# Optimization experiments

Measured on AMD Instinct MI355X. Metric: run time of the kernel, lower is better.

Reference implementation:

```python
import jax, jax.numpy as jnp
import numpy as np
from jax import lax

B, T, I, H, L = 256, 4096, 6, 64, 4


def setup_inputs() -> dict:
    key = jax.random.key(0)
    ks = jax.random.split(key, 8)
    s = 1.0 / np.sqrt(H)  # PyTorch LSTM init scale
    return {
        "x": jax.random.normal(ks[0], (B, T, I), jnp.float32),
        "Wih0": jax.random.uniform(ks[1], (4 * H, I), jnp.float32, -s, s),
        "Wih_rest": jax.random.uniform(ks[2], (L - 1, 4 * H, H), jnp.float32, -s, s),
        "Whh": jax.random.uniform(ks[3], (L, 4 * H, H), jnp.float32, -s, s),
        "bih": jax.random.uniform(ks[4], (L, 4 * H), jnp.float32, -s, s),
        "bhh": jax.random.uniform(ks[5], (L, 4 * H), jnp.float32, -s, s),
        "fc_w": jax.random.uniform(ks[6], (1, H), jnp.float32, -s, s),
        "fc_b": jax.random.uniform(ks[7], (1,), jnp.float32, -s, s),
    }


def _lstm_layer(seq_tbi, Wih_l, Whh_l, b_l):
    # seq_tbi: [T, B, in], time-major. Precompute input projections for all t.
    gx = jnp.einsum('tbi,gi->tbg', seq_tbi, Wih_l) + b_l  # [T, B, 4H]
    batch = seq_tbi.shape[1]
    h0 = jnp.zeros((batch, H), seq_tbi.dtype)
    c0 = jnp.zeros((batch, H), seq_tbi.dtype)

    def step(carry, gxt):
        h, c = carry
        g = gxt + h @ Whh_l.T  # [B, 4H]
        i, f, gg, o = jnp.split(g, 4, axis=-1)  # PyTorch gate order: i,f,g,o
        c = jax.nn.sigmoid(f) * c + jax.nn.sigmoid(i) * jnp.tanh(gg)
        h = jax.nn.sigmoid(o) * jnp.tanh(c)
        return (h, c), h

    _, ys = lax.scan(step, (h0, c0), gx)
    return ys  # [T, B, H]


def reference(x, Wih0, Wih_rest, Whh, bih, bhh, fc_w, fc_b):
    # x: [B, T, I] (batch_first). Dropout(0.2) between layers is inactive (eval).
    seq = jnp.transpose(x, (1, 0, 2))  # time-major [T, B, I]
    for l in range(L):
        Wih_l = Wih0 if l == 0 else Wih_rest[l - 1]
        seq = _lstm_layer(seq, Wih_l, Whh[l], bih[l] + bhh[l])
    last = seq[-1]                      # out[:, -1, :] -> [B, H]
    out = jax.nn.relu(last) @ fc_w.T + fc_b  # [B, 1]
    return out
```

## Files before the change

### kernel.cpp

```cpp
#include <hip/hip_runtime.h>
#include <cstddef>

#define BB 256
#define TT 4096
#define HH 64
#define NT 256
#define CH 8
#define NCH (TT / CH)
#define NGB 16
#define LOG2E 1.442695041f

typedef __attribute__((ext_vector_type(8))) short short8;
typedef __attribute__((ext_vector_type(4))) short short4v;
typedef __attribute__((ext_vector_type(4))) float floatx4;

__device__ int g_flags[3 * NGB];
__global__ void zero_flags_kernel() { g_flags[threadIdx.x] = 0; }

__device__ __forceinline__ floatx4 mfma16(short8 a, short8 b, floatx4 c) {
    return __builtin_amdgcn_mfma_f32_16x16x32_bf16(a, b, c, 0, 0, 0);
}
__device__ __forceinline__ float frcp(float x) { return __builtin_amdgcn_rcpf(x); }
__device__ __forceinline__ void lds_barrier() {
    asm volatile("s_waitcnt lgkmcnt(0)\n\ts_barrier" ::: "memory");
}
__device__ __forceinline__ void bf16split(float v, short& hi, short& lo) {
    unsigned u  = __float_as_uint(v);
    unsigned hu = u & 0xffff0000u;
    hi = (short)(hu >> 16);
    float r = v - __uint_as_float(hu);
    lo = (short)(__float_as_uint(r) >> 16);
}

__global__ __attribute__((amdgpu_flat_work_group_size(NT, NT), amdgpu_waves_per_eu(1)))
void lstm_mfma(const float* __restrict__ xg,
               const float* __restrict__ Wih0,
               const float* __restrict__ WihR,
               const float* __restrict__ Whh4,
               const float* __restrict__ bih4,
               const float* __restrict__ bhh4,
               float* __restrict__ seq)
{
    const int bid = blockIdx.x;
    const int l   = bid >> 4;
    const int gb  = bid & 15;
    const int b0  = gb << 4;
    const bool FIRST = (l == 0);
    const bool LAST  = (l == 3);
    const float* Wih = FIRST ? Wih0 : (WihR + (size_t)(l - 1) * 256 * HH);
    const float* Whh = Whh4 + (size_t)l * 256 * HH;
    int* const fin  = &g_flags[(l - 1) * NGB + gb];
    int* const fout = &g_flags[l * NGB + gb];

    const int tid = threadIdx.x;
    const int w   = tid >> 6;
    const int ln  = tid & 63;
    const int n   = ln & 15;
    const int g4  = ln >> 4;
    const int k0  = (w << 4) + (g4 << 2);

    __shared__ __align__(16) unsigned short xhi[2][CH][16][72];
    __shared__ __align__(16) unsigned short xlo[2][CH][16][72];
    __shared__ __align__(16) unsigned short hhi[2][16][72];
    __shared__ __align__(16) unsigned short hlo[2][16][72];

    short8 whi[4][4], wlo[4][4];
#pragma unroll
    for (int q = 0; q < 4; ++q) {
        const float sc = (q == 2) ? (-2.f * LOG2E) : (-LOG2E);
        const int gr = (q << 6) + (w << 4) + n;
#pragma unroll
        for (int s = 0; s < 4; ++s) {
            const int kb = s * 32 + g4 * 8;
            float wv[8];
#pragma unroll
            for (int i = 0; i < 8; ++i) {
                const int k = kb + i;
                float v;
                if (k < 64)      v = Whh[gr * 64 + k];
                else if (!FIRST) v = Wih[gr * 64 + (k - 64)];
                else             v = (k - 64 < 6) ? Wih[gr * 6 + (k - 64)] : 0.f;
                wv[i] = v * sc;
            }
            short8 hi, lo;
#pragma unroll
            for (int i = 0; i < 8; ++i) { short a, b2; bf16split(wv[i], a, b2); hi[i] = a; lo[i] = b2; }
            whi[q][s] = hi; wlo[q][s] = lo;
        }
    }
    floatx4 bias[4];
#pragma unroll
    for (int q = 0; q < 4; ++q) {
        const float sc = (q == 2) ? (-2.f * LOG2E) : (-LOG2E);
#pragma unroll
        for (int r = 0; r < 4; ++r) {
            const int gr = (q << 6) + k0 + r;
            bias[q][r] = (bih4[l * 256 + gr] + bhh4[l * 256 + gr]) * sc;
        }
    }

    {
        unsigned short* p0 = &xhi[0][0][0][0];
        for (int i = tid; i < 2 * CH * 16 * 72; i += NT) { p0[i] = 0; (&xlo[0][0][0][0])[i] = 0; }
        unsigned short* p1 = &hhi[0][0][0];
        for (int i = tid; i < 2 * 16 * 72; i += NT) { p1[i] = 0; (&hlo[0][0][0])[i] = 0; }
    }
    __syncthreads();

    const int tt = tid >> 5;
    const int sn = (tid >> 1) & 15;
    const int kh = (tid & 1) * 32;
    const int ttf = tid >> 4;
    const int nf  = tid & 15;

    if (!FIRST) {
        if (tid == 0)
            while (__hip_atomic_load(fin, __ATOMIC_ACQUIRE, __HIP_MEMORY_SCOPE_AGENT) < 1)
                __builtin_amdgcn_s_sleep(8);
        __syncthreads();
        const float* src = seq + ((size_t)(0 * CH + tt) * BB + b0 + sn) * HH + kh;
        floatx4 pv[8];
#pragma unroll
        for (int m = 0; m < 8; ++m) pv[m] = ((const floatx4*)src)[m];
#pragma unroll
        for (int m = 0; m < 4; ++m) {
            short8 hi8, lo8;
#pragma unroll
            for (int i = 0; i < 8; ++i) {
                const float v = (i < 4) ? pv[2 * m][i] : pv[2 * m + 1][i - 4];
                short a, b2; bf16split(v, a, b2); hi8[i] = a; lo8[i] = b2;
            }
            *(short8*)&xhi[0][tt][sn][kh + 8 * m] = hi8;
            *(short8*)&xlo[0][tt][sn][kh + 8 * m] = lo8;
        }
    } else if (tid < 128) {
        const float* sx = xg + ((size_t)(b0 + nf) * TT + ttf) * 6;
#pragma unroll
        for (int i = 0; i < 6; ++i) {
            short a, b2; bf16split(sx[i], a, b2);
            xhi[0][ttf][nf][i] = (unsigned short)a;
            xlo[0][ttf][nf][i] = (unsigned short)b2;
        }
    }
    float c0 = 0.f, c1 = 0.f, c2 = 0.f, c3 = 0.f;
    __syncthreads();

    for (int ck = 0; ck < NCH; ++ck) {
        const int buf = ck & 1;
        const bool pfv = (ck + 1 < NCH);
        if (!FIRST && pfv) {
            if (tid == 0)
                while (__hip_atomic_load(fin, __ATOMIC_ACQUIRE, __HIP_MEMORY_SCOPE_AGENT) < ck + 2)
                    __builtin_amdgcn_s_sleep(8);
            __syncthreads();
        }
        floatx4 pv[8];
        float xv[6];

#pragma unroll
        for (int ph = 0; ph < CH; ++ph) {
            const int t = ck * CH + ph;
            if (ph == 0 && pfv) {
                if (!FIRST) {
                    const float* src = seq + ((size_t)((ck + 1) * CH + tt) * BB + b0 + sn) * HH + kh;
#pragma unroll
                    for (int m = 0; m < 8; ++m) pv[m] = ((const floatx4*)src)[m];
                } else if (tid < 128) {
                    const float* sx = xg + ((size_t)(b0 + nf) * TT + (ck + 1) * CH + ttf) * 6;
#pragma unroll
                    for (int i = 0; i < 6; ++i) xv[i] = sx[i];
                }
            }

            const int hb = (t + 1) & 1;
            const short8 bh0 = *(const short8*)&hhi[hb][n][g4 * 8];
            const short8 bh1 = *(const short8*)&hhi[hb][n][32 + g4 * 8];
            const short8 bl0 = *(const short8*)&hlo[hb][n][g4 * 8];
            const short8 bl1 = *(const short8*)&hlo[hb][n][32 + g4 * 8];
            const short8 bx0 = *(const short8*)&xhi[buf][ph][n][g4 * 8];
            const short8 bx1 = *(const short8*)&xhi[buf][ph][n][32 + g4 * 8];
            const short8 by0 = *(const short8*)&xlo[buf][ph][n][g4 * 8];
            const short8 by1 = *(const short8*)&xlo[buf][ph][n][32 + g4 * 8];

            floatx4 a0 = bias[0], a1 = bias[1], a2 = bias[2], a3 = bias[3];
#define TERM(bq0, bq1, bq2, bq3, W) \
            a0 = mfma16(W[0][0], bq0, a0); a1 = mfma16(W[1][0], bq0, a1); \
            a2 = mfma16(W[2][0], bq0, a2); a3 = mfma16(W[3][0], bq0, a3); \
            a0 = mfma16(W[0][1], bq1, a0); a1 = mfma16(W[1][1], bq1, a1); \
            a2 = mfma16(W[2][1], bq1, a2); a3 = mfma16(W[3][1], bq1, a3); \
            a0 = mfma16(W[0][2], bq2, a0); a1 = mfma16(W[1][2], bq2, a1); \
            a2 = mfma16(W[2][2], bq2, a2); a3 = mfma16(W[3][2], bq2, a3); \
            a0 = mfma16(W[0][3], bq3, a0); a1 = mfma16(W[1][3], bq3, a1); \
            a2 = mfma16(W[2][3], bq3, a2); a3 = mfma16(W[3][3], bq3, a3);
            TERM(bh0, bh1, bx0, bx1, whi)
            TERM(bl0, bl1, by0, by1, whi)
            TERM(bh0, bh1, bx0, bx1, wlo)
#undef TERM

            floatx4 hv4;
            short4v h4hi, h4lo;
#define UNIT(r, cr) { \
            const float si = frcp(1.f + exp2f(a0[r])); \
            const float sf = frcp(1.f + exp2f(a1[r])); \
            const float tg = fmaf(2.f, frcp(1.f + exp2f(a2[r])), -1.f); \
            const float so = frcp(1.f + exp2f(a3[r])); \
            cr = fmaf(sf, cr, si * tg); \
            const float tc = fmaf(2.f, frcp(1.f + exp2f(cr * (-2.f * LOG2E))), -1.f); \
            const float hv = so * tc; \
            hv4[r] = hv; \
            short ha, hbs; bf16split(hv, ha, hbs); h4hi[r] = ha; h4lo[r] = hbs; }
            UNIT(0, c0) UNIT(1, c1) UNIT(2, c2) UNIT(3, c3)
#undef UNIT

            *(short4v*)&hhi[t & 1][n][k0] = h4hi;
            *(short4v*)&hlo[t & 1][n][k0] = h4lo;
            if (!LAST || t == TT - 1)
                *(floatx4*)(seq + ((size_t)t * BB + b0 + n) * HH + k0) = hv4;

            if (pfv) {
                if (!FIRST) {
                    if (ph >= 4) {
                        const int m = ph - 4;
                        short8 hi8, lo8;
#pragma unroll
                        for (int i = 0; i < 8; ++i) {
                            const float v = (i < 4) ? pv[2 * m][i] : pv[2 * m + 1][i - 4];
                            short a, b2; bf16split(v, a, b2); hi8[i] = a; lo8[i] = b2;
                        }
                        *(short8*)&xhi[1 - buf][tt][sn][kh + 8 * m] = hi8;
                        *(short8*)&xlo[1 - buf][tt][sn][kh + 8 * m] = lo8;
                    }
                } else if (ph == 2 && tid < 128) {
#pragma unroll
                    for (int i = 0; i < 6; ++i) {
                        short a, b2; bf16split(xv[i], a, b2);
                        xhi[1 - buf][ttf][nf][i] = (unsigned short)a;
                        xlo[1 - buf][ttf][nf][i] = (unsigned short)b2;
                    }
                }
            }

            if (ph < CH - 1) lds_barrier();
            else             __syncthreads();
        }
        if (!LAST && tid == 0)
            __hip_atomic_store(fout, ck + 1, __ATOMIC_RELEASE, __HIP_MEMORY_SCOPE_AGENT);
    }
}

__global__ __launch_bounds__(256)
void fc_kernel(const float* __restrict__ seq, const float* __restrict__ fcw,
               const float* __restrict__ fcb, float* __restrict__ out)
{
    __shared__ float w[HH];
    const int tid = threadIdx.x;
    if (tid < HH) w[tid] = fcw[tid];
    __syncthreads();
    const float* h = &seq[((size_t)(TT - 1) * BB + tid) * HH];
    float s = fcb[0];
#pragma unroll
    for (int jj = 0; jj < HH; ++jj)
        s = fmaf(fmaxf(h[jj], 0.f), w[jj], s);
    out[tid] = s;
}

extern "C" void kernel_launch(void* const* d_in, const int* in_sizes, int n_in,
                              void* d_out, int out_size, void* d_ws, size_t ws_size,
                              hipStream_t stream) {
    const float* x    = (const float*)d_in[0];
    const float* Wih0 = (const float*)d_in[1];
    const float* WihR = (const float*)d_in[2];
    const float* Whh  = (const float*)d_in[3];
    const float* bih  = (const float*)d_in[4];
    const float* bhh  = (const float*)d_in[5];
    const float* fcw  = (const float*)d_in[6];
    const float* fcb  = (const float*)d_in[7];
    float* out = (float*)d_out;
    float* seq = (float*)d_ws;

    zero_flags_kernel<<<dim3(1), dim3(3 * NGB), 0, stream>>>();
    lstm_mfma<<<dim3(4 * NGB), dim3(NT), 0, stream>>>(x, Wih0, WihR, Whh, bih, bhh, seq);
    fc_kernel<<<dim3(1), dim3(256), 0, stream>>>(seq, fcw, fcb, out);
}
```

Baseline: 4.470 ms.

## Batch input-projection MFMAs for four timesteps ahead of the recurrent chain

Each 8-step chunk is split into two groups of four. For each group the input-projection MFMAs (the x-term products) for all four timesteps are computed up front into accumulators. Only the 24 recurrent h-term MFMAs per step then stay on the serial critical path, which is meant to shorten per-step latency in the recurrence. In exchange, 16 extra floatx4 accumulators (64 VGPRs) stay live across steps, which raises register pressure and may cause spills or lower occupancy.

```diff
diff --git a/kernel.cpp b/kernel.cpp
--- a/kernel.cpp
+++ b/kernel.cpp
@@ -158,90 +158,113 @@
         float xv[6];
 
 #pragma unroll
-        for (int ph = 0; ph < CH; ++ph) {
-            const int t = ck * CH + ph;
-            if (ph == 0 && pfv) {
-                if (!FIRST) {
-                    const float* src = seq + ((size_t)((ck + 1) * CH + tt) * BB + b0 + sn) * HH + kh;
-#pragma unroll
-                    for (int m = 0; m < 8; ++m) pv[m] = ((const floatx4*)src)[m];
-                } else if (tid < 128) {
-                    const float* sx = xg + ((size_t)(b0 + nf) * TT + (ck + 1) * CH + ttf) * 6;
-#pragma unroll
-                    for (int i = 0; i < 6; ++i) xv[i] = sx[i];
-                }
+        for (int scn = 0; scn < 2; ++scn) {
+            floatx4 xacc[4][4];
+#pragma unroll
+            for (int s = 0; s < 4; ++s) {
+                const int ph = scn * 4 + s;
+                const short8 bx0 = *(const short8*)&xhi[buf][ph][n][g4 * 8];
+                const short8 bx1 = *(const short8*)&xhi[buf][ph][n][32 + g4 * 8];
+                const short8 by0 = *(const short8*)&xlo[buf][ph][n][g4 * 8];
+                const short8 by1 = *(const short8*)&xlo[buf][ph][n][32 + g4 * 8];
+                floatx4 q0 = bias[0], q1 = bias[1], q2 = bias[2], q3 = bias[3];
+                q0 = mfma16(whi[0][2], bx0, q0); q1 = mfma16(whi[1][2], bx0, q1);
+                q2 = mfma16(whi[2][2], bx0, q2); q3 = mfma16(whi[3][2], bx0, q3);
+                q0 = mfma16(whi[0][3], bx1, q0); q1 = mfma16(whi[1][3], bx1, q1);
+                q2 = mfma16(whi[2][3], bx1, q2); q3 = mfma16(whi[3][3], bx1, q3);
+                q0 = mfma16(wlo[0][2], bx0, q0); q1 = mfma16(wlo[1][2], bx0, q1);
+                q2 = mfma16(wlo[2][2], bx0, q2); q3 = mfma16(wlo[3][2], bx0, q3);
+                q0 = mfma16(wlo[0][3], bx1, q0); q1 = mfma16(wlo[1][3], bx1, q1);
+                q2 = mfma16(wlo[2][3], bx1, q2); q3 = mfma16(wlo[3][3], bx1, q3);
+                q0 = mfma16(whi[0][2], by0, q0); q1 = mfma16(whi[1][2], by0, q1);
+                q2 = mfma16(whi[2][2], by0, q2); q3 = mfma16(whi[3][2], by0, q3);
+                q0 = mfma16(whi[0][3], by1, q0); q1 = mfma16(whi[1][3], by1, q1);
+                q2 = mfma16(whi[2][3], by1, q2); q3 = mfma16(whi[3][3], by1, q3);
+                xacc[s][0] = q0; xacc[s][1] = q1; xacc[s][2] = q2; xacc[s][3] = q3;
             }
 
-            const int hb = (t + 1) & 1;
-            const short8 bh0 = *(const short8*)&hhi[hb][n][g4 * 8];
-            const short8 bh1 = *(const short8*)&hhi[hb][n][32 + g4 * 8];
-            const short8 bl0 = *(const short8*)&hlo[hb][n][g4 * 8];
-            const short8 bl1 = *(const short8*)&hlo[hb][n][32 + g4 * 8];
-            const short8 bx0 = *(const short8*)&xhi[buf][ph][n][g4 * 8];
-            const short8 bx1 = *(const short8*)&xhi[buf][ph][n][32 + g4 * 8];
-            const short8 by0 = *(const short8*)&xlo[buf][ph][n][g4 * 8];
-            const short8 by1 = *(const short8*)&xlo[buf][ph][n][32 + g4 * 8];
-
-            floatx4 a0 = bias[0], a1 = bias[1], a2 = bias[2], a3 = bias[3];
-#define TERM(bq0, bq1, bq2, bq3, W) \
-            a0 = mfma16(W[0][0], bq0, a0); a1 = mfma16(W[1][0], bq0, a1); \
-            a2 = mfma16(W[2][0], bq0, a2); a3 = mfma16(W[3][0], bq0, a3); \
-            a0 = mfma16(W[0][1], bq1, a0); a1 = mfma16(W[1][1], bq1, a1); \
-            a2 = mfma16(W[2][1], bq1, a2); a3 = mfma16(W[3][1], bq1, a3); \
-            a0 = mfma16(W[0][2], bq2, a0); a1 = mfma16(W[1][2], bq2, a1); \
-            a2 = mfma16(W[2][2], bq2, a2); a3 = mfma16(W[3][2], bq2, a3); \
-            a0 = mfma16(W[0][3], bq3, a0); a1 = mfma16(W[1][3], bq3, a1); \
-            a2 = mfma16(W[2][3], bq3, a2); a3 = mfma16(W[3][3], bq3, a3);
-            TERM(bh0, bh1, bx0, bx1, whi)
-            TERM(bl0, bl1, by0, by1, whi)
-            TERM(bh0, bh1, bx0, bx1, wlo)
-#undef TERM
-
-            floatx4 hv4;
-            short4v h4hi, h4lo;
-#define UNIT(r, cr) { \
-            const float si = frcp(1.f + exp2f(a0[r])); \
-            const float sf = frcp(1.f + exp2f(a1[r])); \
-            const float tg = fmaf(2.f, frcp(1.f + exp2f(a2[r])), -1.f); \
-            const float so = frcp(1.f + exp2f(a3[r])); \
-            cr = fmaf(sf, cr, si * tg); \
-            const float tc = fmaf(2.f, frcp(1.f + exp2f(cr * (-2.f * LOG2E))), -1.f); \
-            const float hv = so * tc; \
-            hv4[r] = hv; \
-            short ha, hbs; bf16split(hv, ha, hbs); h4hi[r] = ha; h4lo[r] = hbs; }
-            UNIT(0, c0) UNIT(1, c1) UNIT(2, c2) UNIT(3, c3)
-#undef UNIT
-
-            *(short4v*)&hhi[t & 1][n][k0] = h4hi;
-            *(short4v*)&hlo[t & 1][n][k0] = h4lo;
-            if (!LAST || t == TT - 1)
-                *(floatx4*)(seq + ((size_t)t * BB + b0 + n) * HH + k0) = hv4;
-
-            if (pfv) {
-                if (!FIRST) {
-                    if (ph >= 4) {
-                        const int m = ph - 4;
-                        short8 hi8, lo8;
-#pragma unroll
-                        for (int i = 0; i < 8; ++i) {
-                            const float v = (i < 4) ? pv[2 * m][i] : pv[2 * m + 1][i - 4];
-                            short a, b2; bf16split(v, a, b2); hi8[i] = a; lo8[i] = b2;
-                        }
-                        *(short8*)&xhi[1 - buf][tt][sn][kh + 8 * m] = hi8;
-                        *(short8*)&xlo[1 - buf][tt][sn][kh + 8 * m] = lo8;
-                    }
-                } else if (ph == 2 && tid < 128) {
-#pragma unroll
-                    for (int i = 0; i < 6; ++i) {
-                        short a, b2; bf16split(xv[i], a, b2);
-                        xhi[1 - buf][ttf][nf][i] = (unsigned short)a;
-                        xlo[1 - buf][ttf][nf][i] = (unsigned short)b2;
+#pragma unroll
+            for (int s = 0; s < 4; ++s) {
+                const int ph = scn * 4 + s;
+                const int t = ck * CH + ph;
+                if (ph == 0 && pfv) {
+                    if (!FIRST) {
+                        const float* src = seq + ((size_t)((ck + 1) * CH + tt) * BB + b0 + sn) * HH + kh;
+#pragma unroll
+                        for (int m = 0; m < 8; ++m) pv[m] = ((const floatx4*)src)[m];
+                    } else if (tid < 128) {
+                        const float* sx = xg + ((size_t)(b0 + nf) * TT + (ck + 1) * CH + ttf) * 6;
+#pragma unroll
+                        for (int i = 0; i < 6; ++i) xv[i] = sx[i];
                     }
                 }
+
+                const int hb = (t + 1) & 1;
+                const short8 bh0 = *(const short8*)&hhi[hb][n][g4 * 8];
+                const short8 bh1 = *(const short8*)&hhi[hb][n][32 + g4 * 8];
+                const short8 bl0 = *(const short8*)&hlo[hb][n][g4 * 8];
+                const short8 bl1 = *(const short8*)&hlo[hb][n][32 + g4 * 8];
+
+                floatx4 a0 = xacc[s][0], a1 = xacc[s][1], a2 = xacc[s][2], a3 = xacc[s][3];
+                a0 = mfma16(whi[0][0], bh0, a0); a1 = mfma16(whi[1][0], bh0, a1);
+                a2 = mfma16(whi[2][0], bh0, a2); a3 = mfma16(whi[3][0], bh0, a3);
+                a0 = mfma16(whi[0][1], bh1, a0); a1 = mfma16(whi[1][1], bh1, a1);
+                a2 = mfma16(whi[2][1], bh1, a2); a3 = mfma16(whi[3][1], bh1, a3);
+                a0 = mfma16(wlo[0][0], bh0, a0); a1 = mfma16(wlo[1][0], bh0, a1);
+                a2 = mfma16(wlo[2][0], bh0, a2); a3 = mfma16(wlo[3][0], bh0, a3);
+                a0 = mfma16(wlo[0][1], bh1, a0); a1 = mfma16(wlo[1][1], bh1, a1);
+                a2 = mfma16(wlo[2][1], bh1, a2); a3 = mfma16(wlo[3][1], bh1, a3);
+                a0 = mfma16(whi[0][0], bl0, a0); a1 = mfma16(whi[1][0], bl0, a1);
+                a2 = mfma16(whi[2][0], bl0, a2); a3 = mfma16(whi[3][0], bl0, a3);
+                a0 = mfma16(whi[0][1], bl1, a0); a1 = mfma16(whi[1][1], bl1, a1);
+                a2 = mfma16(whi[2][1], bl1, a2); a3 = mfma16(whi[3][1], bl1, a3);
+
+                floatx4 hv4;
+                short4v h4hi, h4lo;
+#define UNIT(r, cr) { \
+                const float si = frcp(1.f + exp2f(a0[r])); \
+                const float sf = frcp(1.f + exp2f(a1[r])); \
+                const float tg = fmaf(2.f, frcp(1.f + exp2f(a2[r])), -1.f); \
+                const float so = frcp(1.f + exp2f(a3[r])); \
+                cr = fmaf(sf, cr, si * tg); \
+                const float tc = fmaf(2.f, frcp(1.f + exp2f(cr * (-2.f * LOG2E))), -1.f); \
+                const float hv = so * tc; \
+                hv4[r] = hv; \
+                short ha, hbs; bf16split(hv, ha, hbs); h4hi[r] = ha; h4lo[r] = hbs; }
+                UNIT(0, c0) UNIT(1, c1) UNIT(2, c2) UNIT(3, c3)
+#undef UNIT
+
+                *(short4v*)&hhi[t & 1][n][k0] = h4hi;
+                *(short4v*)&hlo[t & 1][n][k0] = h4lo;
+                if (!LAST || t == TT - 1)
+                    *(floatx4*)(seq + ((size_t)t * BB + b0 + n) * HH + k0) = hv4;
+
+                if (pfv) {
+                    if (!FIRST) {
+                        if (ph >= 4) {
+                            const int m = ph - 4;
+                            short8 hi8, lo8;
+#pragma unroll
+                            for (int i = 0; i < 8; ++i) {
+                                const float v = (i < 4) ? pv[2 * m][i] : pv[2 * m + 1][i - 4];
+                                short a, b2; bf16split(v, a, b2); hi8[i] = a; lo8[i] = b2;
+                            }
+                            *(short8*)&xhi[1 - buf][tt][sn][kh + 8 * m] = hi8;
+                            *(short8*)&xlo[1 - buf][tt][sn][kh + 8 * m] = lo8;
+                        }
+                    } else if (ph == 2 && tid < 128) {
+#pragma unroll
+                        for (int i = 0; i < 6; ++i) {
+                            short a, b2; bf16split(xv[i], a, b2);
+                            xhi[1 - buf][ttf][nf][i] = (unsigned short)a;
+                            xlo[1 - buf][ttf][nf][i] = (unsigned short)b2;
+                        }
+                    }
+                }
+
+                if (ph < CH - 1) lds_barrier();
+                else             __syncthreads();
             }
-
-            if (ph < CH - 1) lds_barrier();
-            else             __syncthreads();
         }
         if (!LAST && tid == 0)
             __hip_atomic_store(fout, ck + 1, __ATOMIC_RELEASE, __HIP_MEMORY_SCOPE_AGENT);
```

New measurement: 4.658 ms. 1.04x slower.

## Pack two 16-sample batch groups per workgroup with 512 threads and halve chunk size

Applied to the files above, without the earlier changes.

Each workgroup now runs two independent 16-batch recurrences (two groups of four waves), cutting the grid from 64 to 32 blocks with two waves per SIMD. The idea is to let one group's MFMA and transcendental latency hide behind the other's on the same CU, since the serial recurrence leaves each SIMD mostly idle. Chunk size drops from 8 to 4 timesteps, and the next-chunk conversion is split into a hi pass and a lo pass on separate phases. The risk is that barriers now synchronize both groups together, and register pressure rises with two waves per EU, which could slow each step.

```diff
diff --git a/kernel.cpp b/kernel.cpp
--- a/kernel.cpp
+++ b/kernel.cpp
@@ -4,17 +4,17 @@
 #define BB 256
 #define TT 4096
 #define HH 64
-#define NT 256
-#define CH 8
+#define NT 512
+#define CH 4
 #define NCH (TT / CH)
-#define NGB 16
+#define NPAIR 8
 #define LOG2E 1.442695041f
 
 typedef __attribute__((ext_vector_type(8))) short short8;
 typedef __attribute__((ext_vector_type(4))) short short4v;
 typedef __attribute__((ext_vector_type(4))) float floatx4;
 
-__device__ int g_flags[3 * NGB];
+__device__ int g_flags[3 * NPAIR];
 __global__ void zero_flags_kernel() { g_flags[threadIdx.x] = 0; }
 
 __device__ __forceinline__ floatx4 mfma16(short8 a, short8 b, floatx4 c) {
@@ -32,7 +32,7 @@
     lo = (short)(__float_as_uint(r) >> 16);
 }
 
-__global__ __attribute__((amdgpu_flat_work_group_size(NT, NT), amdgpu_waves_per_eu(1)))
+__global__ __attribute__((amdgpu_flat_work_group_size(NT, NT), amdgpu_waves_per_eu(2)))
 void lstm_mfma(const float* __restrict__ xg,
                const float* __restrict__ Wih0,
                const float* __restrict__ WihR,
@@ -42,27 +42,29 @@
                float* __restrict__ seq)
 {
     const int bid = blockIdx.x;
-    const int l   = bid >> 4;
-    const int gb  = bid & 15;
-    const int b0  = gb << 4;
+    const int l   = bid >> 3;
+    const int gb  = bid & 7;
     const bool FIRST = (l == 0);
     const bool LAST  = (l == 3);
     const float* Wih = FIRST ? Wih0 : (WihR + (size_t)(l - 1) * 256 * HH);
     const float* Whh = Whh4 + (size_t)l * 256 * HH;
-    int* const fin  = &g_flags[(l - 1) * NGB + gb];
-    int* const fout = &g_flags[l * NGB + gb];
-
-    const int tid = threadIdx.x;
-    const int w   = tid >> 6;
-    const int ln  = tid & 63;
-    const int n   = ln & 15;
-    const int g4  = ln >> 4;
-    const int k0  = (w << 4) + (g4 << 2);
-
-    __shared__ __align__(16) unsigned short xhi[2][CH][16][72];
-    __shared__ __align__(16) unsigned short xlo[2][CH][16][72];
-    __shared__ __align__(16) unsigned short hhi[2][16][72];
-    __shared__ __align__(16) unsigned short hlo[2][16][72];
+    int* const fin  = &g_flags[(l - 1) * NPAIR + gb];
+    int* const fout = &g_flags[l * NPAIR + gb];
+
+    const int tid  = threadIdx.x;
+    const int grp  = tid >> 8;
+    const int tid2 = tid & 255;
+    const int w    = (tid >> 6) & 3;
+    const int ln   = tid & 63;
+    const int n    = ln & 15;
+    const int g4   = ln >> 4;
+    const int k0   = (w << 4) + (g4 << 2);
+    const int b0   = (gb << 5) + (grp << 4);
+
+    __shared__ __align__(16) unsigned short xhi[2][2][CH][16][72];
+    __shared__ __align__(16) unsigned short xlo[2][2][CH][16][72];
+    __shared__ __align__(16) unsigned short hhi[2][2][16][72];
+    __shared__ __align__(16) unsigned short hlo[2][2][16][72];
 
     short8 whi[4][4], wlo[4][4];
 #pragma unroll
@@ -100,46 +102,48 @@
     }
 
     {
-        unsigned short* p0 = &xhi[0][0][0][0];
-        for (int i = tid; i < 2 * CH * 16 * 72; i += NT) { p0[i] = 0; (&xlo[0][0][0][0])[i] = 0; }
-        unsigned short* p1 = &hhi[0][0][0];
-        for (int i = tid; i < 2 * 16 * 72; i += NT) { p1[i] = 0; (&hlo[0][0][0])[i] = 0; }
+        unsigned short* px = &xhi[0][0][0][0][0];
+        unsigned short* py = &xlo[0][0][0][0][0];
+        for (int i = tid; i < 2 * 2 * CH * 16 * 72; i += NT) { px[i] = 0; py[i] = 0; }
+        unsigned short* ph_ = &hhi[0][0][0][0];
+        unsigned short* pl_ = &hlo[0][0][0][0];
+        for (int i = tid; i < 2 * 2 * 16 * 72; i += NT) { ph_[i] = 0; pl_[i] = 0; }
     }
     __syncthreads();
 
-    const int tt = tid >> 5;
-    const int sn = (tid >> 1) & 15;
-    const int kh = (tid & 1) * 32;
-    const int ttf = tid >> 4;
-    const int nf  = tid & 15;
+    const int tt = tid2 >> 6;
+    const int sn = (tid2 >> 2) & 15;
+    const int kh = (tid2 & 3) << 4;
+    const int ttf = tid2 >> 4;
+    const int nf  = tid2 & 15;
 
     if (!FIRST) {
         if (tid == 0)
             while (__hip_atomic_load(fin, __ATOMIC_ACQUIRE, __HIP_MEMORY_SCOPE_AGENT) < 1)
                 __builtin_amdgcn_s_sleep(8);
         __syncthreads();
-        const float* src = seq + ((size_t)(0 * CH + tt) * BB + b0 + sn) * HH + kh;
-        floatx4 pv[8];
-#pragma unroll
-        for (int m = 0; m < 8; ++m) pv[m] = ((const floatx4*)src)[m];
-#pragma unroll
-        for (int m = 0; m < 4; ++m) {
+        const float* src = seq + ((size_t)tt * BB + b0 + sn) * HH + kh;
+        floatx4 pv0[4];
+#pragma unroll
+        for (int m = 0; m < 4; ++m) pv0[m] = ((const floatx4*)src)[m];
+#pragma unroll
+        for (int m = 0; m < 2; ++m) {
             short8 hi8, lo8;
 #pragma unroll
             for (int i = 0; i < 8; ++i) {
-                const float v = (i < 4) ? pv[2 * m][i] : pv[2 * m + 1][i - 4];
+                const float v = (i < 4) ? pv0[2 * m][i] : pv0[2 * m + 1][i - 4];
                 short a, b2; bf16split(v, a, b2); hi8[i] = a; lo8[i] = b2;
             }
-            *(short8*)&xhi[0][tt][sn][kh + 8 * m] = hi8;
-            *(short8*)&xlo[0][tt][sn][kh + 8 * m] = lo8;
-        }
-    } else if (tid < 128) {
+            *(short8*)&xhi[grp][0][tt][sn][kh + 8 * m] = hi8;
+            *(short8*)&xlo[grp][0][tt][sn][kh + 8 * m] = lo8;
+        }
+    } else if (tid2 < 64) {
         const float* sx = xg + ((size_t)(b0 + nf) * TT + ttf) * 6;
 #pragma unroll
         for (int i = 0; i < 6; ++i) {
             short a, b2; bf16split(sx[i], a, b2);
-            xhi[0][ttf][nf][i] = (unsigned short)a;
-            xlo[0][ttf][nf][i] = (unsigned short)b2;
+            xhi[grp][0][ttf][nf][i] = (unsigned short)a;
+            xlo[grp][0][ttf][nf][i] = (unsigned short)b2;
         }
     }
     float c0 = 0.f, c1 = 0.f, c2 = 0.f, c3 = 0.f;
@@ -154,7 +158,7 @@
                     __builtin_amdgcn_s_sleep(8);
             __syncthreads();
         }
-        floatx4 pv[8];
+        floatx4 pv[4];
         float xv[6];
 
 #pragma unroll
@@ -164,23 +168,23 @@
                 if (!FIRST) {
                     const float* src = seq + ((size_t)((ck + 1) * CH + tt) * BB + b0 + sn) * HH + kh;
 #pragma unroll
-                    for (int m = 0; m < 8; ++m) pv[m] = ((const floatx4*)src)[m];
-                } else if (tid < 128) {
+                    for (int m = 0; m < 4; ++m) pv[m] = ((const floatx4*)src)[m];
+                } else if (tid2 < 64) {
                     const float* sx = xg + ((size_t)(b0 + nf) * TT + (ck + 1) * CH + ttf) * 6;
 #pragma unroll
                     for (int i = 0; i < 6; ++i) xv[i] = sx[i];
                 }
             }
 
+            const short8 bx0 = *(const short8*)&xhi[grp][buf][ph][n][g4 * 8];
+            const short8 bx1 = *(const short8*)&xhi[grp][buf][ph][n][32 + g4 * 8];
+            const short8 by0 = *(const short8*)&xlo[grp][buf][ph][n][g4 * 8];
+            const short8 by1 = *(const short8*)&xlo[grp][buf][ph][n][32 + g4 * 8];
             const int hb = (t + 1) & 1;
-            const short8 bh0 = *(const short8*)&hhi[hb][n][g4 * 8];
-            const short8 bh1 = *(const short8*)&hhi[hb][n][32 + g4 * 8];
-            const short8 bl0 = *(const short8*)&hlo[hb][n][g4 * 8];
-            const short8 bl1 = *(const short8*)&hlo[hb][n][32 + g4 * 8];
-            const short8 bx0 = *(const short8*)&xhi[buf][ph][n][g4 * 8];
-            const short8 bx1 = *(const short8*)&xhi[buf][ph][n][32 + g4 * 8];
-            const short8 by0 = *(const short8*)&xlo[buf][ph][n][g4 * 8];
-            const short8 by1 = *(const short8*)&xlo[buf][ph][n][32 + g4 * 8];
+            const short8 bh0 = *(const short8*)&hhi[grp][hb][n][g4 * 8];
+            const short8 bh1 = *(const short8*)&hhi[grp][hb][n][32 + g4 * 8];
+            const short8 bl0 = *(const short8*)&hlo[grp][hb][n][g4 * 8];
+            const short8 bl1 = *(const short8*)&hlo[grp][hb][n][32 + g4 * 8];
 
             floatx4 a0 = bias[0], a1 = bias[1], a2 = bias[2], a3 = bias[3];
 #define TERM(bq0, bq1, bq2, bq3, W) \
@@ -212,30 +216,42 @@
             UNIT(0, c0) UNIT(1, c1) UNIT(2, c2) UNIT(3, c3)
 #undef UNIT
 
-            *(short4v*)&hhi[t & 1][n][k0] = h4hi;
-            *(short4v*)&hlo[t & 1][n][k0] = h4lo;
+            *(short4v*)&hhi[grp][t & 1][n][k0] = h4hi;
+            *(short4v*)&hlo[grp][t & 1][n][k0] = h4lo;
             if (!LAST || t == TT - 1)
                 *(floatx4*)(seq + ((size_t)t * BB + b0 + n) * HH + k0) = hv4;
 
             if (pfv) {
                 if (!FIRST) {
-                    if (ph >= 4) {
-                        const int m = ph - 4;
-                        short8 hi8, lo8;
-#pragma unroll
-                        for (int i = 0; i < 8; ++i) {
-                            const float v = (i < 4) ? pv[2 * m][i] : pv[2 * m + 1][i - 4];
-                            short a, b2; bf16split(v, a, b2); hi8[i] = a; lo8[i] = b2;
+                    if (ph == 1) {
+#pragma unroll
+                        for (int m = 0; m < 2; ++m) {
+                            short8 hi8;
+#pragma unroll
+                            for (int i = 0; i < 8; ++i) {
+                                const float v = (i < 4) ? pv[2 * m][i] : pv[2 * m + 1][i - 4];
+                                short a, b2; bf16split(v, a, b2); hi8[i] = a;
+                            }
+                            *(short8*)&xhi[grp][1 - buf][tt][sn][kh + 8 * m] = hi8;
                         }
-                        *(short8*)&xhi[1 - buf][tt][sn][kh + 8 * m] = hi8;
-                        *(short8*)&xlo[1 - buf][tt][sn][kh + 8 * m] = lo8;
+                    } else if (ph == 2) {
+#pragma unroll
+                        for (int m = 0; m < 2; ++m) {
+                            short8 lo8;
+#pragma unroll
+                            for (int i = 0; i < 8; ++i) {
+                                const float v = (i < 4) ? pv[2 * m][i] : pv[2 * m + 1][i - 4];
+                                short a, b2; bf16split(v, a, b2); lo8[i] = b2;
+                            }
+                            *(short8*)&xlo[grp][1 - buf][tt][sn][kh + 8 * m] = lo8;
+                        }
                     }
-                } else if (ph == 2 && tid < 128) {
+                } else if (ph == 2 && tid2 < 64) {
 #pragma unroll
                     for (int i = 0; i < 6; ++i) {
                         short a, b2; bf16split(xv[i], a, b2);
-                        xhi[1 - buf][ttf][nf][i] = (unsigned short)a;
-                        xlo[1 - buf][ttf][nf][i] = (unsigned short)b2;
+                        xhi[grp][1 - buf][ttf][nf][i] = (unsigned short)a;
+                        xlo[grp][1 - buf][ttf][nf][i] = (unsigned short)b2;
                     }
                 }
             }
@@ -278,7 +294,7 @@
     float* out = (float*)d_out;
     float* seq = (float*)d_ws;
 
-    zero_flags_kernel<<<dim3(1), dim3(3 * NGB), 0, stream>>>();
-    lstm_mfma<<<dim3(4 * NGB), dim3(NT), 0, stream>>>(x, Wih0, WihR, Whh, bih, bhh, seq);
+    zero_flags_kernel<<<dim3(1), dim3(3 * NPAIR), 0, stream>>>();
+    lstm_mfma<<<dim3(4 * NPAIR), dim3(NT), 0, stream>>>(x, Wih0, WihR, Whh, bih, bhh, seq);
     fc_kernel<<<dim3(1), dim3(256), 0, stream>>>(seq, fcw, fcb, out);
 }
```

Measured after the change: 7.733 ms. 1.73x slower.

## Split LSTM batch across 128 groups of two rows per layer

Applied to the files above, without the earlier changes.

Batch rows per block drop from 16 to 2, so the grid grows from 64 to 512 blocks. The time chunk shrinks from 8 to 4 steps, and the waves-per-EU hint rises to 2 so two blocks can share a CU. The MFMA tiles still span 16 columns, but only two carry real data; the rest of the hidden state is written as zeros. This aims to spread work over more CUs, but each block still walks the same serial time chain. It adds per-chunk flag synchronisation, and the lower register budget may cause spills of the resident weights.

```diff
diff --git a/kernel.cpp b/kernel.cpp
--- a/kernel.cpp
+++ b/kernel.cpp
@@ -5,16 +5,16 @@
 #define TT 4096
 #define HH 64
 #define NT 256
-#define CH 8
+#define CH 4
 #define NCH (TT / CH)
-#define NGB 16
+#define NG 128
 #define LOG2E 1.442695041f
 
 typedef __attribute__((ext_vector_type(8))) short short8;
 typedef __attribute__((ext_vector_type(4))) short short4v;
 typedef __attribute__((ext_vector_type(4))) float floatx4;
 
-__device__ int g_flags[3 * NGB];
+__device__ int g_flags[3 * NG];
 __global__ void zero_flags_kernel() { g_flags[threadIdx.x] = 0; }
 
 __device__ __forceinline__ floatx4 mfma16(short8 a, short8 b, floatx4 c) {
@@ -32,7 +32,7 @@
     lo = (short)(__float_as_uint(r) >> 16);
 }
 
-__global__ __attribute__((amdgpu_flat_work_group_size(NT, NT), amdgpu_waves_per_eu(1)))
+__global__ __attribute__((amdgpu_flat_work_group_size(NT, NT), amdgpu_waves_per_eu(2)))
 void lstm_mfma(const float* __restrict__ xg,
                const float* __restrict__ Wih0,
                const float* __restrict__ WihR,
@@ -42,15 +42,15 @@
                float* __restrict__ seq)
 {
     const int bid = blockIdx.x;
-    const int l   = bid >> 4;
-    const int gb  = bid & 15;
-    const int b0  = gb << 4;
+    const int l   = bid >> 7;
+    const int gb  = bid & (NG - 1);
+    const int b0  = gb << 1;
     const bool FIRST = (l == 0);
     const bool LAST  = (l == 3);
     const float* Wih = FIRST ? Wih0 : (WihR + (size_t)(l - 1) * 256 * HH);
     const float* Whh = Whh4 + (size_t)l * 256 * HH;
-    int* const fin  = &g_flags[(l - 1) * NGB + gb];
-    int* const fout = &g_flags[l * NGB + gb];
+    int* const fin  = &g_flags[(l - 1) * NG + gb];
+    int* const fout = &g_flags[l * NG + gb];
 
     const int tid = threadIdx.x;
     const int w   = tid >> 6;
@@ -101,39 +101,34 @@
 
     {
         unsigned short* p0 = &xhi[0][0][0][0];
-        for (int i = tid; i < 2 * CH * 16 * 72; i += NT) { p0[i] = 0; (&xlo[0][0][0][0])[i] = 0; }
-        unsigned short* p1 = &hhi[0][0][0];
-        for (int i = tid; i < 2 * 16 * 72; i += NT) { p1[i] = 0; (&hlo[0][0][0])[i] = 0; }
+        unsigned short* p1 = &xlo[0][0][0][0];
+        for (int i = tid; i < 2 * CH * 16 * 72; i += NT) { p0[i] = 0; p1[i] = 0; }
+        unsigned short* p2 = &hhi[0][0][0];
+        unsigned short* p3 = &hlo[0][0][0];
+        for (int i = tid; i < 2 * 16 * 72; i += NT) { p2[i] = 0; p3[i] = 0; }
     }
     __syncthreads();
 
-    const int tt = tid >> 5;
-    const int sn = (tid >> 1) & 15;
-    const int kh = (tid & 1) * 32;
-    const int ttf = tid >> 4;
-    const int nf  = tid & 15;
+    const int tt = tid >> 6;
+    const int c4 = (tid >> 4) & 3;
+    const int kh = (tid & 15) << 2;
+    const int ttf = tid >> 1;
+    const int nf  = tid & 1;
 
     if (!FIRST) {
         if (tid == 0)
             while (__hip_atomic_load(fin, __ATOMIC_ACQUIRE, __HIP_MEMORY_SCOPE_AGENT) < 1)
                 __builtin_amdgcn_s_sleep(8);
         __syncthreads();
-        const float* src = seq + ((size_t)(0 * CH + tt) * BB + b0 + sn) * HH + kh;
-        floatx4 pv[8];
-#pragma unroll
-        for (int m = 0; m < 8; ++m) pv[m] = ((const floatx4*)src)[m];
-#pragma unroll
-        for (int m = 0; m < 4; ++m) {
-            short8 hi8, lo8;
-#pragma unroll
-            for (int i = 0; i < 8; ++i) {
-                const float v = (i < 4) ? pv[2 * m][i] : pv[2 * m + 1][i - 4];
-                short a, b2; bf16split(v, a, b2); hi8[i] = a; lo8[i] = b2;
-            }
-            *(short8*)&xhi[0][tt][sn][kh + 8 * m] = hi8;
-            *(short8*)&xlo[0][tt][sn][kh + 8 * m] = lo8;
-        }
-    } else if (tid < 128) {
+        if (c4 < 2) {
+            const floatx4 v = *(const floatx4*)(seq + ((size_t)tt * BB + b0 + c4) * HH + kh);
+            short4v hi4, lo4;
+#pragma unroll
+            for (int i = 0; i < 4; ++i) { short a, b2; bf16split(v[i], a, b2); hi4[i] = a; lo4[i] = b2; }
+            *(short4v*)&xhi[0][tt][c4][kh] = hi4;
+            *(short4v*)&xlo[0][tt][c4][kh] = lo4;
+        }
+    } else if (tid < 8) {
         const float* sx = xg + ((size_t)(b0 + nf) * TT + ttf) * 6;
 #pragma unroll
         for (int i = 0; i < 6; ++i) {
@@ -154,7 +149,7 @@
                     __builtin_amdgcn_s_sleep(8);
             __syncthreads();
         }
-        floatx4 pv[8];
+        floatx4 pv;
         float xv[6];
 
 #pragma unroll
@@ -162,25 +157,24 @@
             const int t = ck * CH + ph;
             if (ph == 0 && pfv) {
                 if (!FIRST) {
-                    const float* src = seq + ((size_t)((ck + 1) * CH + tt) * BB + b0 + sn) * HH + kh;
-#pragma unroll
-                    for (int m = 0; m < 8; ++m) pv[m] = ((const floatx4*)src)[m];
-                } else if (tid < 128) {
+                    if (c4 < 2)
+                        pv = *(const floatx4*)(seq + ((size_t)((ck + 1) * CH + tt) * BB + b0 + c4) * HH + kh);
+                } else if (tid < 8) {
                     const float* sx = xg + ((size_t)(b0 + nf) * TT + (ck + 1) * CH + ttf) * 6;
 #pragma unroll
                     for (int i = 0; i < 6; ++i) xv[i] = sx[i];
                 }
             }
 
+            const short8 bx0 = *(const short8*)&xhi[buf][ph][n][g4 * 8];
+            const short8 bx1 = *(const short8*)&xhi[buf][ph][n][32 + g4 * 8];
+            const short8 by0 = *(const short8*)&xlo[buf][ph][n][g4 * 8];
+            const short8 by1 = *(const short8*)&xlo[buf][ph][n][32 + g4 * 8];
             const int hb = (t + 1) & 1;
             const short8 bh0 = *(const short8*)&hhi[hb][n][g4 * 8];
             const short8 bh1 = *(const short8*)&hhi[hb][n][32 + g4 * 8];
             const short8 bl0 = *(const short8*)&hlo[hb][n][g4 * 8];
             const short8 bl1 = *(const short8*)&hlo[hb][n][32 + g4 * 8];
-            const short8 bx0 = *(const short8*)&xhi[buf][ph][n][g4 * 8];
-            const short8 bx1 = *(const short8*)&xhi[buf][ph][n][32 + g4 * 8];
-            const short8 by0 = *(const short8*)&xlo[buf][ph][n][g4 * 8];
-            const short8 by1 = *(const short8*)&xlo[buf][ph][n][32 + g4 * 8];
 
             floatx4 a0 = bias[0], a1 = bias[1], a2 = bias[2], a3 = bias[3];
 #define TERM(bq0, bq1, bq2, bq3, W) \
@@ -212,25 +206,22 @@
             UNIT(0, c0) UNIT(1, c1) UNIT(2, c2) UNIT(3, c3)
 #undef UNIT
 
-            *(short4v*)&hhi[t & 1][n][k0] = h4hi;
-            *(short4v*)&hlo[t & 1][n][k0] = h4lo;
-            if (!LAST || t == TT - 1)
+            const short4v z4s = {0, 0, 0, 0};
+            *(short4v*)&hhi[t & 1][n][k0] = (n < 2) ? h4hi : z4s;
+            *(short4v*)&hlo[t & 1][n][k0] = (n < 2) ? h4lo : z4s;
+            if ((!LAST || t == TT - 1) && n < 2)
                 *(floatx4*)(seq + ((size_t)t * BB + b0 + n) * HH + k0) = hv4;
 
-            if (pfv) {
+            if (pfv && ph == 2) {
                 if (!FIRST) {
-                    if (ph >= 4) {
-                        const int m = ph - 4;
-                        short8 hi8, lo8;
-#pragma unroll
-                        for (int i = 0; i < 8; ++i) {
-                            const float v = (i < 4) ? pv[2 * m][i] : pv[2 * m + 1][i - 4];
-                            short a, b2; bf16split(v, a, b2); hi8[i] = a; lo8[i] = b2;
-                        }
-                        *(short8*)&xhi[1 - buf][tt][sn][kh + 8 * m] = hi8;
-                        *(short8*)&xlo[1 - buf][tt][sn][kh + 8 * m] = lo8;
+                    if (c4 < 2) {
+                        short4v hi4, lo4;
+#pragma unroll
+                        for (int i = 0; i < 4; ++i) { short a, b2; bf16split(pv[i], a, b2); hi4[i] = a; lo4[i] = b2; }
+                        *(short4v*)&xhi[1 - buf][tt][c4][kh] = hi4;
+                        *(short4v*)&xlo[1 - buf][tt][c4][kh] = lo4;
                     }
-                } else if (ph == 2 && tid < 128) {
+                } else if (tid < 8) {
 #pragma unroll
                     for (int i = 0; i < 6; ++i) {
                         short a, b2; bf16split(xv[i], a, b2);
@@ -278,7 +269,7 @@
     float* out = (float*)d_out;
     float* seq = (float*)d_ws;
 
-    zero_flags_kernel<<<dim3(1), dim3(3 * NGB), 0, stream>>>();
-    lstm_mfma<<<dim3(4 * NGB), dim3(NT), 0, stream>>>(x, Wih0, WihR, Whh, bih, bhh, seq);
+    zero_flags_kernel<<<dim3(1), dim3(3 * NG), 0, stream>>>();
+    lstm_mfma<<<dim3(4 * NG), dim3(NT), 0, stream>>>(x, Wih0, WihR, Whh, bih, bhh, seq);
     fc_kernel<<<dim3(1), dim3(256), 0, stream>>>(seq, fcw, fcb, out);
 }
```

Measured after the change: 11.56 ms. 2.59x slower.
